# Kernel optimization log

Measured on AMD Instinct MI355X. Metric: run time of the kernel, lower is better.

The kernel has to match this reference:

```python
import jax, jax.numpy as jnp
import numpy as np

N_NODES = 100000
N_EDGES = 3200000
IN_FEATS = 16
HID_FEATS = 64


def setup_inputs() -> dict:
    key = jax.random.key(0)
    ks = jax.random.split(key, 5)
    x = jax.random.normal(ks[0], (N_NODES, IN_FEATS), dtype=jnp.float32)
    src = jax.random.randint(ks[1], (N_EDGES,), 0, N_NODES, dtype=jnp.int64 if jax.config.jax_enable_x64 else jnp.int32)
    dst = jax.random.randint(ks[2], (N_EDGES,), 0, N_NODES, dtype=jnp.int64 if jax.config.jax_enable_x64 else jnp.int32)
    w1 = jax.random.normal(ks[3], (IN_FEATS, HID_FEATS), dtype=jnp.float32) * (1.0 / np.sqrt(IN_FEATS))
    b1 = jnp.zeros((HID_FEATS,), dtype=jnp.float32)
    w2 = jax.random.normal(ks[4], (HID_FEATS, IN_FEATS), dtype=jnp.float32) * (1.0 / np.sqrt(HID_FEATS))
    b2 = jnp.zeros((IN_FEATS,), dtype=jnp.float32)
    return {"x": x, "src": src, "dst": dst, "w1": w1, "b1": b1, "w2": w2, "b2": b2}


def _graph_conv(x, src, dst, W, b):
    """DGL GraphConv with norm='both': D_in^{-1/2} A D_out^{-1/2} X W + b."""
    n = x.shape[0]
    ones = jnp.ones(src.shape[0], dtype=x.dtype)
    deg_out = jnp.clip(jax.ops.segment_sum(ones, src, num_segments=n), 1.0)  # out-degree of src
    deg_in = jnp.clip(jax.ops.segment_sum(ones, dst, num_segments=n), 1.0)   # in-degree of dst
    h = x * (deg_out ** -0.5)[:, None]                 # [N, F] src-side norm
    agg = jax.ops.segment_sum(h[src], dst, num_segments=n)  # gather + scatter-add over edges
    agg = agg * (deg_in ** -0.5)[:, None]              # dst-side norm
    return agg @ W + b


def _symplectic_J(dim, dtype):
    eye = jnp.eye(dim, dtype=dtype)
    half = dim // 2
    return jnp.concatenate([eye[half:], -eye[:half]], axis=0)  # [dim, dim]


def reference(x, src, dst, w1, b1, w2, b2):
    y = jnp.tanh(_graph_conv(x, src, dst, w1, b1))
    y = _graph_conv(y, src, dst, w2, b2)        # dH/dx, shape [N, IN_FEATS]
    J = _symplectic_J(y.shape[1], y.dtype)
    return y @ J.T
```

## Files before the change

### kernel.cpp

```cpp
#include <hip/hip_runtime.h>

#define THREADS 256
#define NB_MAX 512
#define BATCH 4096
#define EPT (BATCH / THREADS)
#define SHIFT 8

__global__ void k_hist(const int* __restrict__ src, const int* __restrict__ dst,
                       int* __restrict__ cnt_src, int* __restrict__ cnt_dst, int nE) {
    __shared__ int hs[NB_MAX], hd[NB_MAX];
    for (int i = threadIdx.x; i < NB_MAX; i += THREADS) { hs[i] = 0; hd[i] = 0; }
    __syncthreads();
    int gid = blockIdx.x * blockDim.x + threadIdx.x;
    int stride = gridDim.x * blockDim.x;
    int nE4 = nE >> 2;
    for (int e4 = gid; e4 < nE4; e4 += stride) {
        int4 s4 = ((const int4*)src)[e4];
        int4 d4 = ((const int4*)dst)[e4];
        atomicAdd(&hs[s4.x >> SHIFT], 1);
        atomicAdd(&hs[s4.y >> SHIFT], 1);
        atomicAdd(&hs[s4.z >> SHIFT], 1);
        atomicAdd(&hs[s4.w >> SHIFT], 1);
        atomicAdd(&hd[d4.x >> SHIFT], 1);
        atomicAdd(&hd[d4.y >> SHIFT], 1);
        atomicAdd(&hd[d4.z >> SHIFT], 1);
        atomicAdd(&hd[d4.w >> SHIFT], 1);
    }
    for (int e = (nE4 << 2) + gid; e < nE; e += stride) {
        atomicAdd(&hs[src[e] >> SHIFT], 1);
        atomicAdd(&hd[dst[e] >> SHIFT], 1);
    }
    __syncthreads();
    for (int i = threadIdx.x; i < NB_MAX; i += THREADS) {
        int a = hs[i], b = hd[i];
        if (a) atomicAdd(&cnt_src[i], a);
        if (b) atomicAdd(&cnt_dst[i], b);
    }
}

__global__ void k_bscan(const int* __restrict__ cnt_src, const int* __restrict__ cnt_dst,
                        int* __restrict__ base_src, int* __restrict__ cur_src,
                        int* __restrict__ base_dst, int* __restrict__ cur_dst) {
    __shared__ int wsA[4], wsB[4];
    int t = threadIdx.x, lane = t & 63, wid = t >> 6;
    int a0 = cnt_src[2*t], a1 = cnt_src[2*t+1];
    int b0 = cnt_dst[2*t], b1 = cnt_dst[2*t+1];
    int sa = a0 + a1, sb = b0 + b1;
    int ia = sa, ib = sb;
#pragma unroll
    for (int off = 1; off < 64; off <<= 1) {
        int va = __shfl_up(ia, off, 64);
        int vb = __shfl_up(ib, off, 64);
        if (lane >= off) { ia += va; ib += vb; }
    }
    if (lane == 63) { wsA[wid] = ia; wsB[wid] = ib; }
    __syncthreads();
    int wa = 0, wb = 0;
    for (int w = 0; w < wid; ++w) { wa += wsA[w]; wb += wsB[w]; }
    int ea = wa + ia - sa, eb = wb + ib - sb;
    base_src[2*t] = ea;      base_src[2*t+1] = ea + a0;
    cur_src[2*t]  = ea;      cur_src[2*t+1]  = ea + a0;
    base_dst[2*t] = eb;      base_dst[2*t+1] = eb + b0;
    cur_dst[2*t]  = eb;      cur_dst[2*t+1]  = eb + b0;
}

__global__ __launch_bounds__(THREADS) void k_bucket_both(
    const int* __restrict__ src, const int* __restrict__ dst,
    int* __restrict__ cur_dst, int* __restrict__ cur_src,
    unsigned int* __restrict__ pairs, unsigned char* __restrict__ psrc, int nE)
{
    __shared__ int base_d[NB_MAX], gbase_d[NB_MAX], cnt2_d[NB_MAX];
    __shared__ int base_s[NB_MAX], gbase_s[NB_MAX], cnt2_s[NB_MAX];
    __shared__ int wsA[4], wsB[4];
    __shared__ unsigned int   st_p[BATCH];
    __shared__ unsigned short st_bd[BATCH];
    __shared__ unsigned char  st_s[BATCH];
    __shared__ unsigned short st_bs[BATCH];

    int t = threadIdx.x;
    int bstart = blockIdx.x * BATCH;
    int bcount = min(BATCH, nE - bstart);

    for (int i = t; i < NB_MAX; i += THREADS) {
        base_d[i] = 0; cnt2_d[i] = 0;
        base_s[i] = 0; cnt2_s[i] = 0;
    }
    __syncthreads();

    int sv[EPT], dv[EPT];
#pragma unroll
    for (int i = 0; i < EPT; ++i) {
        int j = i * THREADS + t;
        if (j < bcount) {
            sv[i] = src[bstart + j];
            dv[i] = dst[bstart + j];
            atomicAdd(&base_d[dv[i] >> SHIFT], 1);
            atomicAdd(&base_s[sv[i] >> SHIFT], 1);
        }
    }
    __syncthreads();

    int hd0 = base_d[2*t], hd1 = base_d[2*t+1];
    int hs0 = base_s[2*t], hs1 = base_s[2*t+1];
    int sd = hd0 + hd1, ss = hs0 + hs1;
    int lane = t & 63, wid = t >> 6;
    int id_ = sd, is_ = ss;
#pragma unroll
    for (int off = 1; off < 64; off <<= 1) {
        int vd = __shfl_up(id_, off, 64);
        int vs = __shfl_up(is_, off, 64);
        if (lane >= off) { id_ += vd; is_ += vs; }
    }
    if (lane == 63) { wsA[wid] = id_; wsB[wid] = is_; }
    __syncthreads();
    int wd = 0, ws_ = 0;
    for (int w = 0; w < wid; ++w) { wd += wsA[w]; ws_ += wsB[w]; }
    int excl_d = wd + id_ - sd;
    int excl_s = ws_ + is_ - ss;
    if (hd0 > 0) gbase_d[2*t]   = atomicAdd(&cur_dst[2*t],   hd0);
    if (hd1 > 0) gbase_d[2*t+1] = atomicAdd(&cur_dst[2*t+1], hd1);
    if (hs0 > 0) gbase_s[2*t]   = atomicAdd(&cur_src[2*t],   hs0);
    if (hs1 > 0) gbase_s[2*t+1] = atomicAdd(&cur_src[2*t+1], hs1);
    base_d[2*t] = excl_d;  base_d[2*t+1] = excl_d + hd0;
    base_s[2*t] = excl_s;  base_s[2*t+1] = excl_s + hs0;
    __syncthreads();

#pragma unroll
    for (int i = 0; i < EPT; ++i) {
        int j = i * THREADS + t;
        if (j < bcount) {
            int d = dv[i], s = sv[i];
            int bd = d >> SHIFT, bs = s >> SHIFT;
            int pd = base_d[bd] + atomicAdd(&cnt2_d[bd], 1);
            st_p[pd]  = ((unsigned int)s << SHIFT) | ((unsigned int)d & 255u);
            st_bd[pd] = (unsigned short)bd;
            int ps = base_s[bs] + atomicAdd(&cnt2_s[bs], 1);
            st_s[ps]  = (unsigned char)(s & 255);
            st_bs[ps] = (unsigned short)bs;
        }
    }
    __syncthreads();

    for (int j = t; j < bcount; j += THREADS) {
        int bd = st_bd[j];
        pairs[gbase_d[bd] + (j - base_d[bd])] = st_p[j];
        int bs = st_bs[j];
        psrc[gbase_s[bs] + (j - base_s[bs])] = st_s[j];
    }
}

__global__ __launch_bounds__(THREADS) void k_count_src(
    const unsigned char* __restrict__ psrc, const int* __restrict__ base_src,
    const int* __restrict__ cnt_src, const float* __restrict__ x,
    float* __restrict__ rsq_out, float* __restrict__ xs, int nN)
{
    __shared__ int c[256];
    int t = threadIdx.x, b = blockIdx.x;
    c[t] = 0;
    __syncthreads();
    int start = base_src[b], end = start + cnt_src[b];
    for (int e = start + t; e < end; e += THREADS)
        atomicAdd(&c[psrc[e]], 1);
    __syncthreads();
    int n = (b << SHIFT) + t;
    if (n < nN) {
        int cc = c[t];
        float ro = rsqrtf((float)(cc > 1 ? cc : 1));
        rsq_out[n] = ro;
        const float4* x4 = (const float4*)(x + (size_t)n * 16);
        float4* xs4 = (float4*)(xs + (size_t)n * 16);
#pragma unroll
        for (int k = 0; k < 4; ++k) {
            float4 v = x4[k];
            v.x *= ro; v.y *= ro; v.z *= ro; v.w *= ro;
            xs4[k] = v;
        }
    }
}

__global__ __launch_bounds__(THREADS) void k_bin_dst(
    const unsigned int* __restrict__ pairs, const int* __restrict__ base_dst,
    const int* __restrict__ cnt_dst, int* __restrict__ deg_in,
    float* __restrict__ rsq_in, int* __restrict__ row_start,
    int* __restrict__ csr_src, int nN)
{
    __shared__ int c[256];
    __shared__ int cur[256];
    __shared__ int wsum[4];
    int t = threadIdx.x, b = blockIdx.x;
    c[t] = 0;
    __syncthreads();
    int start = base_dst[b], end = start + cnt_dst[b];
    for (int e = start + t; e < end; e += THREADS)
        atomicAdd(&c[pairs[e] & 255u], 1);
    __syncthreads();
    int cc = c[t];
    int lane = t & 63, wid = t >> 6;
    int incl = cc;
#pragma unroll
    for (int off = 1; off < 64; off <<= 1) {
        int v = __shfl_up(incl, off, 64);
        if (lane >= off) incl += v;
    }
    if (lane == 63) wsum[wid] = incl;
    __syncthreads();
    int woff = 0;
    for (int w = 0; w < wid; ++w) woff += wsum[w];
    int rs = start + woff + incl - cc;
    cur[t] = rs;
    int n = (b << SHIFT) + t;
    if (n < nN) {
        deg_in[n] = cc;
        rsq_in[n] = rsqrtf((float)(cc > 1 ? cc : 1));
        row_start[n] = rs;
    }
    __syncthreads();
    for (int e = start + t; e < end; e += THREADS) {
        unsigned int pr = pairs[e];
        int pos = atomicAdd(&cur[pr & 255u], 1);
        csr_src[pos] = (int)(pr >> SHIFT);
    }
}

__global__ void k_agg1(const int* __restrict__ row_start, const int* __restrict__ deg_in,
                       const int* __restrict__ csr_src, const float* __restrict__ feat,
                       float* __restrict__ agg, int nN) {
    int tid = blockIdx.x * blockDim.x + threadIdx.x;
    int n = tid >> 2, q = tid & 3;
    if (n >= nN) return;
    int row = row_start[n], deg = deg_in[n];
    const float* fb = feat + q * 4;
    float4 acc = make_float4(0.f, 0.f, 0.f, 0.f);
    int i = 0;
    for (; i + 4 <= deg; i += 4) {
        int s0 = csr_src[row + i];
        int s1 = csr_src[row + i + 1];
        int s2 = csr_src[row + i + 2];
        int s3 = csr_src[row + i + 3];
        float4 v0 = *(const float4*)(fb + (size_t)s0 * 16);
        float4 v1 = *(const float4*)(fb + (size_t)s1 * 16);
        float4 v2 = *(const float4*)(fb + (size_t)s2 * 16);
        float4 v3 = *(const float4*)(fb + (size_t)s3 * 16);
        acc.x += v0.x + v1.x + v2.x + v3.x;
        acc.y += v0.y + v1.y + v2.y + v3.y;
        acc.z += v0.z + v1.z + v2.z + v3.z;
        acc.w += v0.w + v1.w + v2.w + v3.w;
    }
    for (; i < deg; ++i) {
        int s0 = csr_src[row + i];
        float4 v0 = *(const float4*)(fb + (size_t)s0 * 16);
        acc.x += v0.x; acc.y += v0.y; acc.z += v0.z; acc.w += v0.w;
    }
    ((float4*)agg)[(size_t)n * 4 + q] = acc;
}

__global__ __launch_bounds__(THREADS) void k_mlp(
    const float* __restrict__ agg1, const float* __restrict__ rsq_in,
    const float* __restrict__ rsq_out, const float* __restrict__ w1,
    const float* __restrict__ b1, const float* __restrict__ w2,
    float* __restrict__ z, int nN)
{
    int n = blockIdx.x * blockDim.x + threadIdx.x;
    if (n >= nN) return;
    float ri = rsq_in[n];
    const float4* a4 = (const float4*)(agg1 + (size_t)n * 16);
    float t[16];
#pragma unroll
    for (int k = 0; k < 4; ++k) {
        float4 v = a4[k];
        t[4*k+0] = v.x * ri; t[4*k+1] = v.y * ri;
        t[4*k+2] = v.z * ri; t[4*k+3] = v.w * ri;
    }
    float u[16];
#pragma unroll
    for (int o = 0; o < 16; ++o) u[o] = 0.f;
#pragma unroll
    for (int c = 0; c < 4; ++c) {
        float yv[16];
#pragma unroll
        for (int jj = 0; jj < 16; ++jj) yv[jj] = b1[c*16 + jj];
#pragma unroll
        for (int i = 0; i < 16; ++i) {
            float ti = t[i];
#pragma unroll
            for (int jj = 0; jj < 16; ++jj)
                yv[jj] = fmaf(ti, w1[i*64 + c*16 + jj], yv[jj]);
        }
#pragma unroll
        for (int jj = 0; jj < 16; ++jj) {
            float e = __expf(2.f * yv[jj]);
            yv[jj] = 1.f - 2.f * __builtin_amdgcn_rcpf(e + 1.f);
        }
#pragma unroll
        for (int jj = 0; jj < 16; ++jj) {
            float yj = yv[jj];
#pragma unroll
            for (int o = 0; o < 16; ++o)
                u[o] = fmaf(yj, w2[(c*16 + jj)*16 + o], u[o]);
        }
    }
    float ro = rsq_out[n];
    float4* z4 = (float4*)(z + (size_t)n * 16);
#pragma unroll
    for (int k = 0; k < 4; ++k)
        z4[k] = make_float4(u[4*k+0]*ro, u[4*k+1]*ro, u[4*k+2]*ro, u[4*k+3]*ro);
}

__global__ void k_agg2(const int* __restrict__ row_start, const int* __restrict__ deg_in,
                       const int* __restrict__ csr_src, const float* __restrict__ feat,
                       const float* __restrict__ rsq_in, const float* __restrict__ b2,
                       float* __restrict__ out, int nN) {
    int tid = blockIdx.x * blockDim.x + threadIdx.x;
    int n = tid >> 2, q = tid & 3;
    if (n >= nN) return;
    int row = row_start[n], deg = deg_in[n];
    const float* fb = feat + q * 4;
    float4 acc = make_float4(0.f, 0.f, 0.f, 0.f);
    int i = 0;
    for (; i + 4 <= deg; i += 4) {
        int s0 = csr_src[row + i];
        int s1 = csr_src[row + i + 1];
        int s2 = csr_src[row + i + 2];
        int s3 = csr_src[row + i + 3];
        float4 v0 = *(const float4*)(fb + (size_t)s0 * 16);
        float4 v1 = *(const float4*)(fb + (size_t)s1 * 16);
        float4 v2 = *(const float4*)(fb + (size_t)s2 * 16);
        float4 v3 = *(const float4*)(fb + (size_t)s3 * 16);
        acc.x += v0.x + v1.x + v2.x + v3.x;
        acc.y += v0.y + v1.y + v2.y + v3.y;
        acc.z += v0.z + v1.z + v2.z + v3.z;
        acc.w += v0.w + v1.w + v2.w + v3.w;
    }
    for (; i < deg; ++i) {
        int s0 = csr_src[row + i];
        float4 v0 = *(const float4*)(fb + (size_t)s0 * 16);
        acc.x += v0.x; acc.y += v0.y; acc.z += v0.z; acc.w += v0.w;
    }
    float ri = rsq_in[n];
    float4 bq = *(const float4*)(b2 + q * 4);
    float4 g = make_float4(fmaf(acc.x, ri, bq.x), fmaf(acc.y, ri, bq.y),
                           fmaf(acc.z, ri, bq.z), fmaf(acc.w, ri, bq.w));
    float4 p;
    p.x = __shfl_xor(g.x, 2, 64);
    p.y = __shfl_xor(g.y, 2, 64);
    p.z = __shfl_xor(g.z, 2, 64);
    p.w = __shfl_xor(g.w, 2, 64);
    float sgn = (q < 2) ? 1.f : -1.f;
    ((float4*)out)[(size_t)n * 4 + q] =
        make_float4(sgn * p.x, sgn * p.y, sgn * p.z, sgn * p.w);
}

extern "C" void kernel_launch(void* const* d_in, const int* in_sizes, int n_in,
                              void* d_out, int out_size, void* d_ws, size_t ws_size,
                              hipStream_t stream) {
    const float* x  = (const float*)d_in[0];
    const int*   src = (const int*)d_in[1];
    const int*   dst = (const int*)d_in[2];
    const float* w1 = (const float*)d_in[3];
    const float* b1 = (const float*)d_in[4];
    const float* w2 = (const float*)d_in[5];
    const float* b2 = (const float*)d_in[6];
    float* out = (float*)d_out;

    const int nN = in_sizes[0] / 16;
    const int nE = in_sizes[1];
    const int NB = (nN + (1 << SHIFT) - 1) >> SHIFT;

    char* ws = (char*)d_ws;
    size_t off = 0;
    auto carve = [&](size_t bytes) -> void* {
        void* p = ws + off;
        off += (bytes + 255) & ~(size_t)255;
        return p;
    };
    int* cnt_src = (int*)carve((size_t)2 * NB_MAX * sizeof(int));
    int* cnt_dst = cnt_src + NB_MAX;
    int* base_src = (int*)carve((size_t)NB_MAX * sizeof(int));
    int* cur_src  = (int*)carve((size_t)NB_MAX * sizeof(int));
    int* base_dst = (int*)carve((size_t)NB_MAX * sizeof(int));
    int* cur_dst  = (int*)carve((size_t)NB_MAX * sizeof(int));
    float* rsq_out  = (float*)carve((size_t)nN * sizeof(float));
    float* rsq_in   = (float*)carve((size_t)nN * sizeof(float));
    int*   row_start = (int*)carve((size_t)nN * sizeof(int));
    int*   deg_in    = (int*)carve((size_t)nN * sizeof(int));
    float* xs   = (float*)carve((size_t)nN * 16 * sizeof(float));
    int*   csr_src = (int*)carve((size_t)nE * sizeof(int));
    unsigned char* psrc = (unsigned char*)carve((size_t)nE);
    size_t un_sz = (size_t)nE * 4 > (size_t)nN * 64 ? (size_t)nE * 4 : (size_t)nN * 64;
    void* un = carve(un_sz);
    unsigned int* pairs = (unsigned int*)un;
    float* agg1 = (float*)un;

    const int node_blocks = (nN + THREADS - 1) / THREADS;
    const int quad_blocks = (4 * nN + THREADS - 1) / THREADS;
    const int batch_blocks = (nE + BATCH - 1) / BATCH;

    hipMemsetAsync(cnt_src, 0, (size_t)2 * NB_MAX * sizeof(int), stream);
    k_hist<<<256, THREADS, 0, stream>>>(src, dst, cnt_src, cnt_dst, nE);
    k_bscan<<<1, THREADS, 0, stream>>>(cnt_src, cnt_dst, base_src, cur_src, base_dst, cur_dst);
    k_bucket_both<<<batch_blocks, THREADS, 0, stream>>>(src, dst, cur_dst, cur_src,
                                                        pairs, psrc, nE);
    k_count_src<<<NB, THREADS, 0, stream>>>(psrc, base_src, cnt_src, x, rsq_out, xs, nN);
    k_bin_dst<<<NB, THREADS, 0, stream>>>(pairs, base_dst, cnt_dst, deg_in, rsq_in,
                                          row_start, csr_src, nN);
    k_agg1<<<quad_blocks, THREADS, 0, stream>>>(row_start, deg_in, csr_src, xs, agg1, nN);
    k_mlp<<<node_blocks, THREADS, 0, stream>>>(agg1, rsq_in, rsq_out, w1, b1, w2, xs, nN);
    k_agg2<<<quad_blocks, THREADS, 0, stream>>>(row_start, deg_in, csr_src, xs,
                                                rsq_in, b2, out, nN);
}
```

Before: 317.9 us.

## Vectorize bucket scatter, drop per-element bucket ids, unroll aggregation gathers by eight

The bucketing kernel now loads src/dst as int4 and reuses the bucket base counters as running slot cursors, which removes the separate count arrays. The per-element bucket id arrays are replaced by a coarse binary-search lookup table, indexed per 16 elements, followed by a short linear scan. This cuts LDS usage and should raise occupancy. Both aggregation kernels add an 8-way unrolled gather loop with two accumulators to keep more loads in flight, and the histogram kernel grid is doubled. The changes add lookup overhead in the write-out loop and slightly reorder floating-point summation.

```diff
diff --git a/kernel.cpp b/kernel.cpp
--- a/kernel.cpp
+++ b/kernel.cpp
@@ -4,6 +4,7 @@
 #define NB_MAX 512
 #define BATCH 4096
 #define EPT (BATCH / THREADS)
+#define EPT4 (EPT / 4)
 #define SHIFT 8
 
 __global__ void k_hist(const int* __restrict__ src, const int* __restrict__ dst,
@@ -69,34 +70,46 @@
     int* __restrict__ cur_dst, int* __restrict__ cur_src,
     unsigned int* __restrict__ pairs, unsigned char* __restrict__ psrc, int nE)
 {
-    __shared__ int base_d[NB_MAX], gbase_d[NB_MAX], cnt2_d[NB_MAX];
-    __shared__ int base_s[NB_MAX], gbase_s[NB_MAX], cnt2_s[NB_MAX];
+    __shared__ int base_d[NB_MAX], gbase_d[NB_MAX];
+    __shared__ int base_s[NB_MAX], gbase_s[NB_MAX];
     __shared__ int wsA[4], wsB[4];
-    __shared__ unsigned int   st_p[BATCH];
-    __shared__ unsigned short st_bd[BATCH];
-    __shared__ unsigned char  st_s[BATCH];
-    __shared__ unsigned short st_bs[BATCH];
+    __shared__ unsigned int  st_p[BATCH];
+    __shared__ unsigned char st_s[BATCH];
+    __shared__ unsigned short jb_d[BATCH / 16], jb_s[BATCH / 16];
 
     int t = threadIdx.x;
     int bstart = blockIdx.x * BATCH;
     int bcount = min(BATCH, nE - bstart);
-
-    for (int i = t; i < NB_MAX; i += THREADS) {
-        base_d[i] = 0; cnt2_d[i] = 0;
-        base_s[i] = 0; cnt2_s[i] = 0;
-    }
-    __syncthreads();
-
-    int sv[EPT], dv[EPT];
-#pragma unroll
-    for (int i = 0; i < EPT; ++i) {
-        int j = i * THREADS + t;
-        if (j < bcount) {
-            sv[i] = src[bstart + j];
-            dv[i] = dst[bstart + j];
-            atomicAdd(&base_d[dv[i] >> SHIFT], 1);
-            atomicAdd(&base_s[sv[i] >> SHIFT], 1);
-        }
+    int n4 = bcount >> 2;
+    int tail = bcount - (n4 << 2);
+
+    for (int i = t; i < NB_MAX; i += THREADS) { base_d[i] = 0; base_s[i] = 0; }
+    __syncthreads();
+
+    int4 sv4[EPT4], dv4[EPT4];
+    int sv_t = 0, dv_t = 0;
+    bool have_t = (t < tail);
+#pragma unroll
+    for (int i = 0; i < EPT4; ++i) {
+        int q = i * THREADS + t;
+        if (q < n4) {
+            sv4[i] = ((const int4*)(src + bstart))[q];
+            dv4[i] = ((const int4*)(dst + bstart))[q];
+            atomicAdd(&base_s[sv4[i].x >> SHIFT], 1);
+            atomicAdd(&base_s[sv4[i].y >> SHIFT], 1);
+            atomicAdd(&base_s[sv4[i].z >> SHIFT], 1);
+            atomicAdd(&base_s[sv4[i].w >> SHIFT], 1);
+            atomicAdd(&base_d[dv4[i].x >> SHIFT], 1);
+            atomicAdd(&base_d[dv4[i].y >> SHIFT], 1);
+            atomicAdd(&base_d[dv4[i].z >> SHIFT], 1);
+            atomicAdd(&base_d[dv4[i].w >> SHIFT], 1);
+        }
+    }
+    if (have_t) {
+        sv_t = src[bstart + (n4 << 2) + t];
+        dv_t = dst[bstart + (n4 << 2) + t];
+        atomicAdd(&base_s[sv_t >> SHIFT], 1);
+        atomicAdd(&base_d[dv_t >> SHIFT], 1);
     }
     __syncthreads();
 
@@ -126,26 +139,49 @@
     __syncthreads();
 
 #pragma unroll
-    for (int i = 0; i < EPT; ++i) {
-        int j = i * THREADS + t;
-        if (j < bcount) {
-            int d = dv[i], s = sv[i];
-            int bd = d >> SHIFT, bs = s >> SHIFT;
-            int pd = base_d[bd] + atomicAdd(&cnt2_d[bd], 1);
-            st_p[pd]  = ((unsigned int)s << SHIFT) | ((unsigned int)d & 255u);
-            st_bd[pd] = (unsigned short)bd;
-            int ps = base_s[bs] + atomicAdd(&cnt2_s[bs], 1);
-            st_s[ps]  = (unsigned char)(s & 255);
-            st_bs[ps] = (unsigned short)bs;
-        }
+    for (int i = 0; i < EPT4; ++i) {
+        int q = i * THREADS + t;
+        if (q < n4) {
+            int ss4[4] = { sv4[i].x, sv4[i].y, sv4[i].z, sv4[i].w };
+            int dd4[4] = { dv4[i].x, dv4[i].y, dv4[i].z, dv4[i].w };
+#pragma unroll
+            for (int k = 0; k < 4; ++k) {
+                int s = ss4[k], d = dd4[k];
+                int pd = atomicAdd(&base_d[d >> SHIFT], 1);
+                st_p[pd] = ((unsigned int)s << SHIFT) | ((unsigned int)d & 255u);
+                int ps = atomicAdd(&base_s[s >> SHIFT], 1);
+                st_s[ps] = (unsigned char)(s & 255);
+            }
+        }
+    }
+    if (have_t) {
+        int pd = atomicAdd(&base_d[dv_t >> SHIFT], 1);
+        st_p[pd] = ((unsigned int)sv_t << SHIFT) | ((unsigned int)dv_t & 255u);
+        int ps = atomicAdd(&base_s[sv_t >> SHIFT], 1);
+        st_s[ps] = (unsigned char)(sv_t & 255);
+    }
+    __syncthreads();
+
+    {
+        int target = t << 4;
+        int lo = 0, hi = NB_MAX;
+        while (lo < hi) { int mid = (lo + hi) >> 1; if (base_d[mid] > target) hi = mid; else lo = mid + 1; }
+        jb_d[t] = (unsigned short)lo;
+        lo = 0; hi = NB_MAX;
+        while (lo < hi) { int mid = (lo + hi) >> 1; if (base_s[mid] > target) hi = mid; else lo = mid + 1; }
+        jb_s[t] = (unsigned short)lo;
     }
     __syncthreads();
 
     for (int j = t; j < bcount; j += THREADS) {
-        int bd = st_bd[j];
-        pairs[gbase_d[bd] + (j - base_d[bd])] = st_p[j];
-        int bs = st_bs[j];
-        psrc[gbase_s[bs] + (j - base_s[bs])] = st_s[j];
+        int b = jb_d[j >> 4];
+        while (base_d[b] <= j) ++b;
+        int ob = b ? base_d[b - 1] : 0;
+        pairs[gbase_d[b] + (j - ob)] = st_p[j];
+        int c = jb_s[j >> 4];
+        while (base_s[c] <= j) ++c;
+        int oc = c ? base_s[c - 1] : 0;
+        psrc[gbase_s[c] + (j - oc)] = st_s[j];
     }
 }
 
@@ -231,7 +267,24 @@
     int row = row_start[n], deg = deg_in[n];
     const float* fb = feat + q * 4;
     float4 acc = make_float4(0.f, 0.f, 0.f, 0.f);
+    float4 acc2 = make_float4(0.f, 0.f, 0.f, 0.f);
     int i = 0;
+    for (; i + 8 <= deg; i += 8) {
+        int s[8];
+#pragma unroll
+        for (int k = 0; k < 8; ++k) s[k] = csr_src[row + i + k];
+        float4 v[8];
+#pragma unroll
+        for (int k = 0; k < 8; ++k) v[k] = *(const float4*)(fb + (size_t)s[k] * 16);
+        acc.x  += v[0].x + v[1].x + v[2].x + v[3].x;
+        acc.y  += v[0].y + v[1].y + v[2].y + v[3].y;
+        acc.z  += v[0].z + v[1].z + v[2].z + v[3].z;
+        acc.w  += v[0].w + v[1].w + v[2].w + v[3].w;
+        acc2.x += v[4].x + v[5].x + v[6].x + v[7].x;
+        acc2.y += v[4].y + v[5].y + v[6].y + v[7].y;
+        acc2.z += v[4].z + v[5].z + v[6].z + v[7].z;
+        acc2.w += v[4].w + v[5].w + v[6].w + v[7].w;
+    }
     for (; i + 4 <= deg; i += 4) {
         int s0 = csr_src[row + i];
         int s1 = csr_src[row + i + 1];
@@ -251,6 +304,7 @@
         float4 v0 = *(const float4*)(fb + (size_t)s0 * 16);
         acc.x += v0.x; acc.y += v0.y; acc.z += v0.z; acc.w += v0.w;
     }
+    acc.x += acc2.x; acc.y += acc2.y; acc.z += acc2.z; acc.w += acc2.w;
     ((float4*)agg)[(size_t)n * 4 + q] = acc;
 }
 
@@ -316,7 +370,24 @@
     int row = row_start[n], deg = deg_in[n];
     const float* fb = feat + q * 4;
     float4 acc = make_float4(0.f, 0.f, 0.f, 0.f);
+    float4 acc2 = make_float4(0.f, 0.f, 0.f, 0.f);
     int i = 0;
+    for (; i + 8 <= deg; i += 8) {
+        int s[8];
+#pragma unroll
+        for (int k = 0; k < 8; ++k) s[k] = csr_src[row + i + k];
+        float4 v[8];
+#pragma unroll
+        for (int k = 0; k < 8; ++k) v[k] = *(const float4*)(fb + (size_t)s[k] * 16);
+        acc.x  += v[0].x + v[1].x + v[2].x + v[3].x;
+        acc.y  += v[0].y + v[1].y + v[2].y + v[3].y;
+        acc.z  += v[0].z + v[1].z + v[2].z + v[3].z;
+        acc.w  += v[0].w + v[1].w + v[2].w + v[3].w;
+        acc2.x += v[4].x + v[5].x + v[6].x + v[7].x;
+        acc2.y += v[4].y + v[5].y + v[6].y + v[7].y;
+        acc2.z += v[4].z + v[5].z + v[6].z + v[7].z;
+        acc2.w += v[4].w + v[5].w + v[6].w + v[7].w;
+    }
     for (; i + 4 <= deg; i += 4) {
         int s0 = csr_src[row + i];
         int s1 = csr_src[row + i + 1];
@@ -336,6 +407,7 @@
         float4 v0 = *(const float4*)(fb + (size_t)s0 * 16);
         acc.x += v0.x; acc.y += v0.y; acc.z += v0.z; acc.w += v0.w;
     }
+    acc.x += acc2.x; acc.y += acc2.y; acc.z += acc2.z; acc.w += acc2.w;
     float ri = rsq_in[n];
     float4 bq = *(const float4*)(b2 + q * 4);
     float4 g = make_float4(fmaf(acc.x, ri, bq.x), fmaf(acc.y, ri, bq.y),
@@ -396,7 +468,7 @@
     const int batch_blocks = (nE + BATCH - 1) / BATCH;
 
     hipMemsetAsync(cnt_src, 0, (size_t)2 * NB_MAX * sizeof(int), stream);
-    k_hist<<<256, THREADS, 0, stream>>>(src, dst, cnt_src, cnt_dst, nE);
+    k_hist<<<512, THREADS, 0, stream>>>(src, dst, cnt_src, cnt_dst, nE);
     k_bscan<<<1, THREADS, 0, stream>>>(cnt_src, cnt_dst, base_src, cur_src, base_dst, cur_dst);
     k_bucket_both<<<batch_blocks, THREADS, 0, stream>>>(src, dst, cur_dst, cur_src,
                                                         pairs, psrc, nE);
```

Result: faster. 309.2 us (-2.8%).
